# Kernel tuning notes

Measured on AMD Instinct MI355X. Metric: run time of the kernel, lower is better.

Reference implementation:

```python
import jax, jax.numpy as jnp
import numpy as np

SPARSITY = 0.9  # target fraction of zeros (magnitude pruning)
D_IN = 4096
D_OUT = 4096
TOKENS = 4096


def setup_inputs() -> dict:
    key = jax.random.key(0)
    k1, k2 = jax.random.split(key)
    x = jax.random.normal(k1, (TOKENS, D_IN), dtype=jnp.float32)
    weight = jax.random.normal(k2, (D_OUT, D_IN), dtype=jnp.float32) * 0.01
    bias = jnp.zeros((D_OUT,), dtype=jnp.float32)
    return {"x": x, "weight": weight, "bias": bias}


def reference(x, weight, bias):
    # Magnitude pruning: threshold at the SPARSITY quantile of |W|,
    # keep only entries strictly above threshold (matches CSR build),
    # then sparse-dense GEMM y = x @ W_pruned^T + b.
    aw = jnp.abs(weight)
    thr = jnp.quantile(aw, SPARSITY)
    w_pruned = jnp.where(aw > thr, weight, jnp.zeros_like(weight))
    return x @ w_pruned.T + bias
```

## Files before the change

kernel.cpp:

```cpp
#include <hip/hip_runtime.h>
#include <stdint.h>

#define D_IN   4096
#define D_OUT  4096
#define NTOK   4096
#define NW     (D_OUT * D_IN)
#define RANK1  15099493u

typedef unsigned int  uint32;
typedef unsigned short ushort_t;
typedef float  f32x4  __attribute__((ext_vector_type(4)));
typedef __bf16 bf16x8 __attribute__((ext_vector_type(8)));

__device__ __forceinline__ uint32 rne_bf16(float f) {
  uint32 u = __float_as_uint(f);
  return (u + 0x7FFFu + ((u >> 16) & 1u)) >> 16;
}

__device__ __forceinline__ void gload_lds16(const void* g, void* l) {
  __builtin_amdgcn_global_load_lds((__attribute__((address_space(1))) void*)(g),
                                   (__attribute__((address_space(3))) void*)(l), 16, 0, 0);
}

__global__ void hist_pass1(const uint4* __restrict__ wb, uint32* __restrict__ hist) {
  __shared__ uint32 lh[4][2048];
  for (int i = threadIdx.x; i < 8192; i += 256) ((uint32*)lh)[i] = 0;
  __syncthreads();
  int wid = threadIdx.x >> 6;
  int idx = blockIdx.x * 256 + threadIdx.x;
  int stride = gridDim.x * 256;
  for (int i = idx; i < NW / 4; i += stride) {
    uint4 v = wb[i];
    atomicAdd(&lh[wid][(v.x & 0x7FFFFFFFu) >> 20], 1u);
    atomicAdd(&lh[wid][(v.y & 0x7FFFFFFFu) >> 20], 1u);
    atomicAdd(&lh[wid][(v.z & 0x7FFFFFFFu) >> 20], 1u);
    atomicAdd(&lh[wid][(v.w & 0x7FFFFFFFu) >> 20], 1u);
  }
  __syncthreads();
  for (int i = threadIdx.x; i < 2048; i += 256) {
    uint32 c = lh[0][i] + lh[1][i] + lh[2][i] + lh[3][i];
    if (c) atomicAdd(&hist[i], c);
  }
}

__global__ void hist_pass23(const uint4* __restrict__ wb, const uint32* __restrict__ state,
                            uint32* __restrict__ hist, int pass) {
  __shared__ uint32 lh[1024];
  for (int i = threadIdx.x; i < 1024; i += 256) lh[i] = 0;
  __syncthreads();
  uint32 pref = state[pass == 2 ? 0 : 2];
  int fsh = (pass == 2) ? 20 : 10;
  int bsh = (pass == 2) ? 10 : 0;
  int idx = blockIdx.x * 256 + threadIdx.x;
  int stride = gridDim.x * 256;
  for (int i = idx; i < NW / 4; i += stride) {
    uint4 v = wb[i];
    uint32 k;
    k = v.x & 0x7FFFFFFFu; if ((k >> fsh) == pref) atomicAdd(&lh[(k >> bsh) & 1023u], 1u);
    k = v.y & 0x7FFFFFFFu; if ((k >> fsh) == pref) atomicAdd(&lh[(k >> bsh) & 1023u], 1u);
    k = v.z & 0x7FFFFFFFu; if ((k >> fsh) == pref) atomicAdd(&lh[(k >> bsh) & 1023u], 1u);
    k = v.w & 0x7FFFFFFFu; if ((k >> fsh) == pref) atomicAdd(&lh[(k >> bsh) & 1023u], 1u);
  }
  __syncthreads();
  for (int i = threadIdx.x; i < 1024; i += 256) { uint32 c = lh[i]; if (c) atomicAdd(&hist[i], c); }
}

__global__ void scan_select(const uint32* __restrict__ hist, int nbins,
                            uint32* __restrict__ state, int pass) {
  int tid = threadIdx.x;
  int per = nbins >> 8;
  uint32 loc[8];
  uint32 s = 0;
  int base = tid * per;
  for (int i = 0; i < per; i++) { loc[i] = hist[base + i]; s += loc[i]; }
  int lane = tid & 63, wid = tid >> 6;
  uint32 v = s;
  for (int d = 1; d < 64; d <<= 1) { uint32 o = __shfl_up(v, (unsigned)d); if (lane >= d) v += o; }
  __shared__ uint32 wtot[4];
  if (lane == 63) wtot[wid] = v;
  __syncthreads();
  uint32 woff = 0;
  for (int w = 0; w < wid; w++) woff += wtot[w];
  uint32 incl = v + woff;
  uint32 excl = incl - s;
  uint32 rank = (pass == 1) ? RANK1 : state[(pass == 2) ? 1 : 3];
  if (rank >= excl && rank < incl) {
    uint32 c = excl; int b = base;
    for (int i = 0; i < per; i++) {
      if (rank < c + loc[i]) { b = base + i; break; }
      c += loc[i];
    }
    uint32 rw = rank - c;
    if (pass == 1)      { state[0] = (uint32)b; state[1] = rw; }
    else if (pass == 2) { state[2] = (state[0] << 10) | (uint32)b; state[3] = rw; }
    else                { state[4] = (state[2] << 10) | (uint32)b; }
  }
}

__global__ void convert_w(const float4* __restrict__ w, const uint32* __restrict__ state,
                          uint4* __restrict__ out) {
  float thr = __uint_as_float(state[4]);
  int i = blockIdx.x * 256 + threadIdx.x;
  int stride = gridDim.x * 256;
  for (; i < NW / 8; i += stride) {
    float4 a = w[2 * i], b = w[2 * i + 1];
    float f[8] = {a.x, a.y, a.z, a.w, b.x, b.y, b.z, b.w};
    uint32 h[8];
#pragma unroll
    for (int j = 0; j < 8; j++) h[j] = (fabsf(f[j]) > thr) ? rne_bf16(f[j]) : 0u;
    uint4 o;
    o.x = h[0] | (h[1] << 16);
    o.y = h[2] | (h[3] << 16);
    o.z = h[4] | (h[5] << 16);
    o.w = h[6] | (h[7] << 16);
    out[i] = o;
  }
}

__global__ void convert_x(const float4* __restrict__ x, uint4* __restrict__ out) {
  int i = blockIdx.x * 256 + threadIdx.x;
  int stride = gridDim.x * 256;
  for (; i < NW / 8; i += stride) {
    float4 a = x[2 * i], b = x[2 * i + 1];
    uint4 o;
    o.x = rne_bf16(a.x) | (rne_bf16(a.y) << 16);
    o.y = rne_bf16(a.z) | (rne_bf16(a.w) << 16);
    o.z = rne_bf16(b.x) | (rne_bf16(b.y) << 16);
    o.w = rne_bf16(b.z) | (rne_bf16(b.w) << 16);
    out[i] = o;
  }
}

#define TILES 128

__device__ __forceinline__ void stage16k(const ushort_t* __restrict__ G, int rowbase, int kt,
                                         ushort_t* lbase, int tid) {
#pragma unroll
  for (int j = 0; j < 2; j++) {
    int idx = j * 512 + tid;
    int r = idx >> 2;
    int cl = (idx & 3) ^ ((r >> 1) & 3);
    gload_lds16(G + (size_t)(rowbase + r) * D_IN + kt + cl * 8, lbase + idx * 8);
  }
}

__global__ __launch_bounds__(512, 2) void gemm_bt(const ushort_t* __restrict__ A,
                                                  const ushort_t* __restrict__ B,
                                                  const float* __restrict__ bias,
                                                  float* __restrict__ C) {
  extern __shared__ ushort_t lds[];

  int bid = blockIdx.x;
  int swz = (bid & 7) * 32 + (bid >> 3);
  int bm = swz >> 4;
  int bn = swz & 15;

  int tid  = threadIdx.x;
  int lane = tid & 63;
  int wave = tid >> 6;
  int wm = wave >> 2, wn = wave & 3;

  int l15  = lane & 15;
  int csel = (lane >> 4) ^ ((lane >> 1) & 3);

  const ushort_t* Ag = A;
  const ushort_t* Bg = B;

  f32x4 acc[8][4];
#pragma unroll
  for (int m = 0; m < 8; m++)
#pragma unroll
    for (int n = 0; n < 4; n++) acc[m][n] = (f32x4){0.f, 0.f, 0.f, 0.f};

  stage16k(Ag, bm * 256, 0,  lds,                 tid);
  stage16k(Bg, bn * 256, 0,  lds + 8192,          tid);
  stage16k(Ag, bm * 256, 32, lds + 16384,         tid);
  stage16k(Bg, bn * 256, 32, lds + 16384 + 8192,  tid);
  asm volatile("s_waitcnt vmcnt(4)" ::: "memory");
  asm volatile("s_barrier" ::: "memory");

  int ar = wm * 128 + l15;
  int br = wn * 64 + l15;

  int cur = 0, sd = 2;
  for (int t = 0; t < TILES; t++) {
    int u = t + 2; if (u > TILES - 1) u = TILES - 1;
    int kup = u * 32;
    ushort_t* sbase = lds + sd * 16384;
    const bf16x8* A8 = (const bf16x8*)(lds + cur * 16384);
    const bf16x8* B8 = A8 + 1024;

    bf16x8 af[8], bv[4];
#pragma unroll
    for (int mm = 0; mm < 4; mm++) af[mm] = A8[(ar + mm * 16) * 4 + csel];
#pragma unroll
    for (int n = 0; n < 4; n++)    bv[n] = B8[(br + n * 16) * 4 + csel];
    __builtin_amdgcn_sched_barrier(0);
#pragma unroll
    for (int mm = 4; mm < 8; mm++) af[mm] = A8[(ar + mm * 16) * 4 + csel];
    stage16k(Ag, bm * 256, kup, sbase, tid);
    stage16k(Bg, bn * 256, kup, sbase + 8192, tid);

    asm volatile("s_waitcnt lgkmcnt(4)" ::: "memory");
    __builtin_amdgcn_sched_barrier(0);
    __builtin_amdgcn_s_setprio(1);
#pragma unroll
    for (int mm = 0; mm < 4; mm++)
#pragma unroll
      for (int n = 0; n < 4; n++)
        acc[mm][n] = __builtin_amdgcn_mfma_f32_16x16x32_bf16(af[mm], bv[n], acc[mm][n], 0, 0, 0);
    __builtin_amdgcn_s_setprio(0);

    asm volatile("s_waitcnt lgkmcnt(0)" ::: "memory");
    __builtin_amdgcn_sched_barrier(0);
    __builtin_amdgcn_s_setprio(1);
#pragma unroll
    for (int mm = 4; mm < 8; mm++)
#pragma unroll
      for (int n = 0; n < 4; n++)
        acc[mm][n] = __builtin_amdgcn_mfma_f32_16x16x32_bf16(af[mm], bv[n], acc[mm][n], 0, 0, 0);
    __builtin_amdgcn_s_setprio(0);
    __builtin_amdgcn_sched_barrier(0);

    asm volatile("s_waitcnt vmcnt(4)" ::: "memory");
    asm volatile("s_barrier" ::: "memory");

    cur = (cur == 2) ? 0 : cur + 1;
    sd  = (sd  == 2) ? 0 : sd + 1;
  }

  int orow0 = bm * 256 + wm * 128 + (lane >> 4) * 4;
  int ocol0 = bn * 256 + wn * 64 + l15;
#pragma unroll
  for (int n = 0; n < 4; n++) {
    float bv2 = bias[ocol0 + n * 16];
#pragma unroll
    for (int m = 0; m < 8; m++) {
#pragma unroll
      for (int r = 0; r < 4; r++) {
        C[(size_t)(orow0 + m * 16 + r) * D_OUT + ocol0 + n * 16] = acc[m][n][r] + bv2;
      }
    }
  }
}

extern "C" void kernel_launch(void* const* d_in, const int* in_sizes, int n_in,
                              void* d_out, int out_size, void* d_ws, size_t ws_size,
                              hipStream_t stream) {
  const float* x = (const float*)d_in[0];
  const float* w = (const float*)d_in[1];
  const float* bias = (const float*)d_in[2];
  float* out = (float*)d_out;

  char* ws = (char*)d_ws;
  uint32* hist1 = (uint32*)ws;
  uint32* hist2 = (uint32*)(ws + 8192);
  uint32* hist3 = (uint32*)(ws + 12288);
  uint32* state = (uint32*)(ws + 16384);
  ushort_t* Xb = (ushort_t*)(ws + 65536);
  ushort_t* Wb = (ushort_t*)(ws + 65536 + (size_t)NW * 2);

  hipMemsetAsync(d_ws, 0, 16448, stream);

  hist_pass1<<<2048, 256, 0, stream>>>((const uint4*)w, hist1);
  scan_select<<<1, 256, 0, stream>>>(hist1, 2048, state, 1);
  hist_pass23<<<2048, 256, 0, stream>>>((const uint4*)w, state, hist2, 2);
  scan_select<<<1, 256, 0, stream>>>(hist2, 1024, state, 2);
  hist_pass23<<<2048, 256, 0, stream>>>((const uint4*)w, state, hist3, 3);
  scan_select<<<1, 256, 0, stream>>>(hist3, 1024, state, 3);

  convert_w<<<2048, 256, 0, stream>>>((const float4*)w, state, (uint4*)Wb);
  convert_x<<<2048, 256, 0, stream>>>((const float4*)x, (uint4*)Xb);

  gemm_bt<<<256, 512, 98304, stream>>>(Xb, Wb, bias, out);
}
```

Before: 257.9 us.

## Fuse select into histogram kernels, merge x conversion, restructure GEMM main loop

```diff
diff --git a/kernel.cpp b/kernel.cpp
--- a/kernel.cpp
+++ b/kernel.cpp
@@ -22,87 +22,120 @@
                                    (__attribute__((address_space(3))) void*)(l), 16, 0, 0);
 }
 
-__global__ void hist_pass1(const uint4* __restrict__ wb, uint32* __restrict__ hist) {
-  __shared__ uint32 lh[4][2048];
-  for (int i = threadIdx.x; i < 8192; i += 256) ((uint32*)lh)[i] = 0;
-  __syncthreads();
-  int wid = threadIdx.x >> 6;
-  int idx = blockIdx.x * 256 + threadIdx.x;
-  int stride = gridDim.x * 256;
-  for (int i = idx; i < NW / 4; i += stride) {
-    uint4 v = wb[i];
-    atomicAdd(&lh[wid][(v.x & 0x7FFFFFFFu) >> 20], 1u);
-    atomicAdd(&lh[wid][(v.y & 0x7FFFFFFFu) >> 20], 1u);
-    atomicAdd(&lh[wid][(v.z & 0x7FFFFFFFu) >> 20], 1u);
-    atomicAdd(&lh[wid][(v.w & 0x7FFFFFFFu) >> 20], 1u);
-  }
-  __syncthreads();
-  for (int i = threadIdx.x; i < 2048; i += 256) {
-    uint32 c = lh[0][i] + lh[1][i] + lh[2][i] + lh[3][i];
-    if (c) atomicAdd(&hist[i], c);
-  }
-}
-
-__global__ void hist_pass23(const uint4* __restrict__ wb, const uint32* __restrict__ state,
-                            uint32* __restrict__ hist, int pass) {
-  __shared__ uint32 lh[1024];
-  for (int i = threadIdx.x; i < 1024; i += 256) lh[i] = 0;
-  __syncthreads();
-  uint32 pref = state[pass == 2 ? 0 : 2];
-  int fsh = (pass == 2) ? 20 : 10;
-  int bsh = (pass == 2) ? 10 : 0;
-  int idx = blockIdx.x * 256 + threadIdx.x;
-  int stride = gridDim.x * 256;
-  for (int i = idx; i < NW / 4; i += stride) {
-    uint4 v = wb[i];
-    uint32 k;
-    k = v.x & 0x7FFFFFFFu; if ((k >> fsh) == pref) atomicAdd(&lh[(k >> bsh) & 1023u], 1u);
-    k = v.y & 0x7FFFFFFFu; if ((k >> fsh) == pref) atomicAdd(&lh[(k >> bsh) & 1023u], 1u);
-    k = v.z & 0x7FFFFFFFu; if ((k >> fsh) == pref) atomicAdd(&lh[(k >> bsh) & 1023u], 1u);
-    k = v.w & 0x7FFFFFFFu; if ((k >> fsh) == pref) atomicAdd(&lh[(k >> bsh) & 1023u], 1u);
-  }
-  __syncthreads();
-  for (int i = threadIdx.x; i < 1024; i += 256) { uint32 c = lh[i]; if (c) atomicAdd(&hist[i], c); }
-}
-
-__global__ void scan_select(const uint32* __restrict__ hist, int nbins,
-                            uint32* __restrict__ state, int pass) {
+template <int NB>
+__device__ __forceinline__ void dsel(const uint32* __restrict__ h, uint32 rank,
+                                     uint32* res, uint32* wtot) {
+  constexpr int PER = NB >> 8;
   int tid = threadIdx.x;
-  int per = nbins >> 8;
-  uint32 loc[8];
+  int lane = tid & 63, wid = tid >> 6;
+  uint32 loc[PER];
   uint32 s = 0;
-  int base = tid * per;
-  for (int i = 0; i < per; i++) { loc[i] = hist[base + i]; s += loc[i]; }
-  int lane = tid & 63, wid = tid >> 6;
+  int base = tid * PER;
+#pragma unroll
+  for (int i = 0; i < PER; i++) { loc[i] = h[base + i]; s += loc[i]; }
   uint32 v = s;
   for (int d = 1; d < 64; d <<= 1) { uint32 o = __shfl_up(v, (unsigned)d); if (lane >= d) v += o; }
-  __shared__ uint32 wtot[4];
   if (lane == 63) wtot[wid] = v;
   __syncthreads();
   uint32 woff = 0;
   for (int w = 0; w < wid; w++) woff += wtot[w];
-  uint32 incl = v + woff;
-  uint32 excl = incl - s;
-  uint32 rank = (pass == 1) ? RANK1 : state[(pass == 2) ? 1 : 3];
+  uint32 incl = v + woff, excl = incl - s;
   if (rank >= excl && rank < incl) {
-    uint32 c = excl; int b = base;
-    for (int i = 0; i < per; i++) {
-      if (rank < c + loc[i]) { b = base + i; break; }
+    uint32 c = excl;
+#pragma unroll
+    for (int i = 0; i < PER; i++) {
+      if (rank < c + loc[i]) { res[0] = (uint32)(base + i); res[1] = rank - c; break; }
       c += loc[i];
     }
-    uint32 rw = rank - c;
-    if (pass == 1)      { state[0] = (uint32)b; state[1] = rw; }
-    else if (pass == 2) { state[2] = (state[0] << 10) | (uint32)b; state[3] = rw; }
-    else                { state[4] = (state[2] << 10) | (uint32)b; }
-  }
-}
-
-__global__ void convert_w(const float4* __restrict__ w, const uint32* __restrict__ state,
-                          uint4* __restrict__ out) {
-  float thr = __uint_as_float(state[4]);
+  }
+  __syncthreads();
+}
+
+__global__ void k1_hist1_convx(const uint4* __restrict__ wb, uint32* __restrict__ hist,
+                               const float4* __restrict__ x, uint4* __restrict__ xout) {
+  __shared__ uint32 lh[4][2048];
+  if (blockIdx.x < 2048) {
+    for (int i = threadIdx.x; i < 8192; i += 256) ((uint32*)lh)[i] = 0;
+    __syncthreads();
+    int wid = threadIdx.x >> 6;
+    int idx = blockIdx.x * 256 + threadIdx.x;
+    for (int i = idx; i < NW / 4; i += 2048 * 256) {
+      uint4 v = wb[i];
+      atomicAdd(&lh[wid][(v.x & 0x7FFFFFFFu) >> 20], 1u);
+      atomicAdd(&lh[wid][(v.y & 0x7FFFFFFFu) >> 20], 1u);
+      atomicAdd(&lh[wid][(v.z & 0x7FFFFFFFu) >> 20], 1u);
+      atomicAdd(&lh[wid][(v.w & 0x7FFFFFFFu) >> 20], 1u);
+    }
+    __syncthreads();
+    for (int i = threadIdx.x; i < 2048; i += 256) {
+      uint32 c = lh[0][i] + lh[1][i] + lh[2][i] + lh[3][i];
+      if (c) atomicAdd(&hist[i], c);
+    }
+  } else {
+    int i = (blockIdx.x - 2048) * 256 + threadIdx.x;
+    for (; i < NW / 8; i += 1024 * 256) {
+      float4 a = x[2 * i], b = x[2 * i + 1];
+      uint4 o;
+      o.x = rne_bf16(a.x) | (rne_bf16(a.y) << 16);
+      o.y = rne_bf16(a.z) | (rne_bf16(a.w) << 16);
+      o.z = rne_bf16(b.x) | (rne_bf16(b.y) << 16);
+      o.w = rne_bf16(b.z) | (rne_bf16(b.w) << 16);
+      xout[i] = o;
+    }
+  }
+}
+
+__global__ void k2_hist2(const uint4* __restrict__ wb, const uint32* __restrict__ hist1,
+                         uint32* __restrict__ hist2) {
+  __shared__ uint32 lh[1024];
+  __shared__ uint32 res1[2], wt[4];
+  for (int i = threadIdx.x; i < 1024; i += 256) lh[i] = 0;
+  dsel<2048>(hist1, RANK1, res1, wt);
+  uint32 pref = res1[0];
+  int idx = blockIdx.x * 256 + threadIdx.x;
+  for (int i = idx; i < NW / 4; i += 2048 * 256) {
+    uint4 v = wb[i];
+    uint32 k;
+    k = v.x & 0x7FFFFFFFu; if ((k >> 20) == pref) atomicAdd(&lh[(k >> 10) & 1023u], 1u);
+    k = v.y & 0x7FFFFFFFu; if ((k >> 20) == pref) atomicAdd(&lh[(k >> 10) & 1023u], 1u);
+    k = v.z & 0x7FFFFFFFu; if ((k >> 20) == pref) atomicAdd(&lh[(k >> 10) & 1023u], 1u);
+    k = v.w & 0x7FFFFFFFu; if ((k >> 20) == pref) atomicAdd(&lh[(k >> 10) & 1023u], 1u);
+  }
+  __syncthreads();
+  for (int i = threadIdx.x; i < 1024; i += 256) { uint32 c = lh[i]; if (c) atomicAdd(&hist2[i], c); }
+}
+
+__global__ void k3_hist3(const uint4* __restrict__ wb, const uint32* __restrict__ hist1,
+                         const uint32* __restrict__ hist2, uint32* __restrict__ hist3) {
+  __shared__ uint32 lh[1024];
+  __shared__ uint32 res1[2], res2[2], wt[4];
+  for (int i = threadIdx.x; i < 1024; i += 256) lh[i] = 0;
+  dsel<2048>(hist1, RANK1, res1, wt);
+  dsel<1024>(hist2, res1[1], res2, wt);
+  uint32 pref = (res1[0] << 10) | res2[0];
+  int idx = blockIdx.x * 256 + threadIdx.x;
+  for (int i = idx; i < NW / 4; i += 2048 * 256) {
+    uint4 v = wb[i];
+    uint32 k;
+    k = v.x & 0x7FFFFFFFu; if ((k >> 10) == pref) atomicAdd(&lh[k & 1023u], 1u);
+    k = v.y & 0x7FFFFFFFu; if ((k >> 10) == pref) atomicAdd(&lh[k & 1023u], 1u);
+    k = v.z & 0x7FFFFFFFu; if ((k >> 10) == pref) atomicAdd(&lh[k & 1023u], 1u);
+    k = v.w & 0x7FFFFFFFu; if ((k >> 10) == pref) atomicAdd(&lh[k & 1023u], 1u);
+  }
+  __syncthreads();
+  for (int i = threadIdx.x; i < 1024; i += 256) { uint32 c = lh[i]; if (c) atomicAdd(&hist3[i], c); }
+}
+
+__global__ void k4_convw(const float4* __restrict__ w, const uint32* __restrict__ hist1,
+                         const uint32* __restrict__ hist2, const uint32* __restrict__ hist3,
+                         uint4* __restrict__ out) {
+  __shared__ uint32 res1[2], res2[2], res3[2], wt[4];
+  dsel<2048>(hist1, RANK1, res1, wt);
+  dsel<1024>(hist2, res1[1], res2, wt);
+  dsel<1024>(hist3, res2[1], res3, wt);
+  float thr = __uint_as_float((res1[0] << 20) | (res2[0] << 10) | res3[0]);
   int i = blockIdx.x * 256 + threadIdx.x;
-  int stride = gridDim.x * 256;
-  for (; i < NW / 8; i += stride) {
+  for (; i < NW / 8; i += 2048 * 256) {
     float4 a = w[2 * i], b = w[2 * i + 1];
     float f[8] = {a.x, a.y, a.z, a.w, b.x, b.y, b.z, b.w};
     uint32 h[8];
@@ -117,32 +150,7 @@
   }
 }
 
-__global__ void convert_x(const float4* __restrict__ x, uint4* __restrict__ out) {
-  int i = blockIdx.x * 256 + threadIdx.x;
-  int stride = gridDim.x * 256;
-  for (; i < NW / 8; i += stride) {
-    float4 a = x[2 * i], b = x[2 * i + 1];
-    uint4 o;
-    o.x = rne_bf16(a.x) | (rne_bf16(a.y) << 16);
-    o.y = rne_bf16(a.z) | (rne_bf16(a.w) << 16);
-    o.z = rne_bf16(b.x) | (rne_bf16(b.y) << 16);
-    o.w = rne_bf16(b.z) | (rne_bf16(b.w) << 16);
-    out[i] = o;
-  }
-}
-
 #define TILES 128
-
-__device__ __forceinline__ void stage16k(const ushort_t* __restrict__ G, int rowbase, int kt,
-                                         ushort_t* lbase, int tid) {
-#pragma unroll
-  for (int j = 0; j < 2; j++) {
-    int idx = j * 512 + tid;
-    int r = idx >> 2;
-    int cl = (idx & 3) ^ ((r >> 1) & 3);
-    gload_lds16(G + (size_t)(rowbase + r) * D_IN + kt + cl * 8, lbase + idx * 8);
-  }
-}
 
 __global__ __launch_bounds__(512, 2) void gemm_bt(const ushort_t* __restrict__ A,
                                                   const ushort_t* __restrict__ B,
@@ -163,8 +171,14 @@
   int l15  = lane & 15;
   int csel = (lane >> 4) ^ ((lane >> 1) & 3);
 
-  const ushort_t* Ag = A;
-  const ushort_t* Bg = B;
+  int idx0 = tid, idx1 = 512 + tid;
+  int sr0 = idx0 >> 2, scl0 = (idx0 & 3) ^ ((sr0 >> 1) & 3);
+  int sr1 = idx1 >> 2, scl1 = (idx1 & 3) ^ ((sr1 >> 1) & 3);
+  int ld0 = idx0 * 8, ld1 = idx1 * 8;
+  const ushort_t* pA0 = A + (size_t)(bm * 256 + sr0) * D_IN + scl0 * 8;
+  const ushort_t* pA1 = A + (size_t)(bm * 256 + sr1) * D_IN + scl1 * 8;
+  const ushort_t* pB0 = B + (size_t)(bn * 256 + sr0) * D_IN + scl0 * 8;
+  const ushort_t* pB1 = B + (size_t)(bn * 256 + sr1) * D_IN + scl1 * 8;
 
   f32x4 acc[8][4];
 #pragma unroll
@@ -172,10 +186,11 @@
 #pragma unroll
     for (int n = 0; n < 4; n++) acc[m][n] = (f32x4){0.f, 0.f, 0.f, 0.f};
 
-  stage16k(Ag, bm * 256, 0,  lds,                 tid);
-  stage16k(Bg, bn * 256, 0,  lds + 8192,          tid);
-  stage16k(Ag, bm * 256, 32, lds + 16384,         tid);
-  stage16k(Bg, bn * 256, 32, lds + 16384 + 8192,  tid);
+  gload_lds16(pA0,      lds + ld0);         gload_lds16(pA1,      lds + ld1);
+  gload_lds16(pB0,      lds + 8192 + ld0);  gload_lds16(pB1,      lds + 8192 + ld1);
+  gload_lds16(pA0 + 32, lds + 16384 + ld0); gload_lds16(pA1 + 32, lds + 16384 + ld1);
+  gload_lds16(pB0 + 32, lds + 24576 + ld0); gload_lds16(pB1 + 32, lds + 24576 + ld1);
+  pA0 += 64; pA1 += 64; pB0 += 64; pB1 += 64;
   asm volatile("s_waitcnt vmcnt(4)" ::: "memory");
   asm volatile("s_barrier" ::: "memory");
 
@@ -184,47 +199,77 @@
 
   int cur = 0, sd = 2;
   for (int t = 0; t < TILES; t++) {
-    int u = t + 2; if (u > TILES - 1) u = TILES - 1;
-    int kup = u * 32;
     ushort_t* sbase = lds + sd * 16384;
     const bf16x8* A8 = (const bf16x8*)(lds + cur * 16384);
     const bf16x8* B8 = A8 + 1024;
 
-    bf16x8 af[8], bv[4];
-#pragma unroll
-    for (int mm = 0; mm < 4; mm++) af[mm] = A8[(ar + mm * 16) * 4 + csel];
-#pragma unroll
-    for (int n = 0; n < 4; n++)    bv[n] = B8[(br + n * 16) * 4 + csel];
-    __builtin_amdgcn_sched_barrier(0);
-#pragma unroll
-    for (int mm = 4; mm < 8; mm++) af[mm] = A8[(ar + mm * 16) * 4 + csel];
-    stage16k(Ag, bm * 256, kup, sbase, tid);
-    stage16k(Bg, bn * 256, kup, sbase + 8192, tid);
+    bf16x8 bv0, bv1, bv2, bv3, a0, a1, a2, a3, a4, a5, a6, a7;
+    bv0 = B8[(br +  0) * 4 + csel];
+    bv1 = B8[(br + 16) * 4 + csel];
+    bv2 = B8[(br + 32) * 4 + csel];
+    bv3 = B8[(br + 48) * 4 + csel];
+    a0  = A8[(ar +  0) * 4 + csel];
+    a1  = A8[(ar + 16) * 4 + csel];
+    __builtin_amdgcn_sched_barrier(0);
+    a2  = A8[(ar + 32) * 4 + csel];
+    a3  = A8[(ar + 48) * 4 + csel];
+    a4  = A8[(ar + 64) * 4 + csel];
+    a5  = A8[(ar + 80) * 4 + csel];
+    a6  = A8[(ar + 96) * 4 + csel];
+    a7  = A8[(ar + 112) * 4 + csel];
+    __builtin_amdgcn_sched_barrier(0);
+    gload_lds16(pA0, sbase + ld0);
+    gload_lds16(pA1, sbase + ld1);
+    gload_lds16(pB0, sbase + 8192 + ld0);
+    gload_lds16(pB1, sbase + 8192 + ld1);
+    __builtin_amdgcn_sched_barrier(0);
+
+    asm volatile("s_waitcnt lgkmcnt(6)" ::: "memory");
+    __builtin_amdgcn_sched_barrier(0);
+    __builtin_amdgcn_s_setprio(1);
+#pragma unroll
+    for (int n = 0; n < 4; n++) {
+      bf16x8 bvv = (n == 0) ? bv0 : (n == 1) ? bv1 : (n == 2) ? bv2 : bv3;
+      acc[0][n] = __builtin_amdgcn_mfma_f32_16x16x32_bf16(a0, bvv, acc[0][n], 0, 0, 0);
+      acc[1][n] = __builtin_amdgcn_mfma_f32_16x16x32_bf16(a1, bvv, acc[1][n], 0, 0, 0);
+    }
+    __builtin_amdgcn_s_setprio(0);
 
     asm volatile("s_waitcnt lgkmcnt(4)" ::: "memory");
     __builtin_amdgcn_sched_barrier(0);
     __builtin_amdgcn_s_setprio(1);
 #pragma unroll
-    for (int mm = 0; mm < 4; mm++)
-#pragma unroll
-      for (int n = 0; n < 4; n++)
-        acc[mm][n] = __builtin_amdgcn_mfma_f32_16x16x32_bf16(af[mm], bv[n], acc[mm][n], 0, 0, 0);
+    for (int n = 0; n < 4; n++) {
+      bf16x8 bvv = (n == 0) ? bv0 : (n == 1) ? bv1 : (n == 2) ? bv2 : bv3;
+      acc[2][n] = __builtin_amdgcn_mfma_f32_16x16x32_bf16(a2, bvv, acc[2][n], 0, 0, 0);
+      acc[3][n] = __builtin_amdgcn_mfma_f32_16x16x32_bf16(a3, bvv, acc[3][n], 0, 0, 0);
+    }
     __builtin_amdgcn_s_setprio(0);
 
-    asm volatile("s_waitcnt lgkmcnt(0)" ::: "memory");
+    asm volatile("s_waitcnt lgkmcnt(2)" ::: "memory");
     __builtin_amdgcn_sched_barrier(0);
     __builtin_amdgcn_s_setprio(1);
 #pragma unroll
-    for (int mm = 4; mm < 8; mm++)
-#pragma unroll
-      for (int n = 0; n < 4; n++)
-        acc[mm][n] = __builtin_amdgcn_mfma_f32_16x16x32_bf16(af[mm], bv[n], acc[mm][n], 0, 0, 0);
+    for (int n = 0; n < 4; n++) {
+      bf16x8 bvv = (n == 0) ? bv0 : (n == 1) ? bv1 : (n == 2) ? bv2 : bv3;
+      acc[4][n] = __builtin_amdgcn_mfma_f32_16x16x32_bf16(a4, bvv, acc[4][n], 0, 0, 0);
+      acc[5][n] = __builtin_amdgcn_mfma_f32_16x16x32_bf16(a5, bvv, acc[5][n], 0, 0, 0);
+    }
     __builtin_amdgcn_s_setprio(0);
-    __builtin_amdgcn_sched_barrier(0);
-
-    asm volatile("s_waitcnt vmcnt(4)" ::: "memory");
+
+    asm volatile("s_waitcnt vmcnt(4) lgkmcnt(0)" ::: "memory");
     asm volatile("s_barrier" ::: "memory");
-
+    __builtin_amdgcn_sched_barrier(0);
+    __builtin_amdgcn_s_setprio(1);
+#pragma unroll
+    for (int n = 0; n < 4; n++) {
+      bf16x8 bvv = (n == 0) ? bv0 : (n == 1) ? bv1 : (n == 2) ? bv2 : bv3;
+      acc[6][n] = __builtin_amdgcn_mfma_f32_16x16x32_bf16(a6, bvv, acc[6][n], 0, 0, 0);
+      acc[7][n] = __builtin_amdgcn_mfma_f32_16x16x32_bf16(a7, bvv, acc[7][n], 0, 0, 0);
+    }
+    __builtin_amdgcn_s_setprio(0);
+
+    if (t < TILES - 3) { pA0 += 32; pA1 += 32; pB0 += 32; pB1 += 32; }
     cur = (cur == 2) ? 0 : cur + 1;
     sd  = (sd  == 2) ? 0 : sd + 1;
   }
@@ -256,21 +301,15 @@
   uint32* hist1 = (uint32*)ws;
   uint32* hist2 = (uint32*)(ws + 8192);
   uint32* hist3 = (uint32*)(ws + 12288);
-  uint32* state = (uint32*)(ws + 16384);
   ushort_t* Xb = (ushort_t*)(ws + 65536);
   ushort_t* Wb = (ushort_t*)(ws + 65536 + (size_t)NW * 2);
 
-  hipMemsetAsync(d_ws, 0, 16448, stream);
-
-  hist_pass1<<<2048, 256, 0, stream>>>((const uint4*)w, hist1);
-  scan_select<<<1, 256, 0, stream>>>(hist1, 2048, state, 1);
-  hist_pass23<<<2048, 256, 0, stream>>>((const uint4*)w, state, hist2, 2);
-  scan_select<<<1, 256, 0, stream>>>(hist2, 1024, state, 2);
-  hist_pass23<<<2048, 256, 0, stream>>>((const uint4*)w, state, hist3, 3);
-  scan_select<<<1, 256, 0, stream>>>(hist3, 1024, state, 3);
-
-  convert_w<<<2048, 256, 0, stream>>>((const float4*)w, state, (uint4*)Wb);
-  convert_x<<<2048, 256, 0, stream>>>((const float4*)x, (uint4*)Xb);
+  hipMemsetAsync(d_ws, 0, 16384, stream);
+
+  k1_hist1_convx<<<3072, 256, 0, stream>>>((const uint4*)w, hist1, (const float4*)x, (uint4*)Xb);
+  k2_hist2<<<2048, 256, 0, stream>>>((const uint4*)w, hist1, hist2);
+  k3_hist3<<<2048, 256, 0, stream>>>((const uint4*)w, hist1, hist2, hist3);
+  k4_convw<<<2048, 256, 0, stream>>>((const float4*)w, hist1, hist2, hist3, (uint4*)Wb);
 
   gemm_bt<<<256, 512, 98304, stream>>>(Xb, Wb, bias, out);
 }
```

Result: faster. 242.1 us (-6.1%).
